# Performance work log

Hardware: AMD Instinct MI355X
Metric: run time of the kernel (lower is better)

Reference implementation:

```python
import jax, jax.numpy as jnp
import numpy as np

M, K, N = 32, 8192, 28672

def setup_inputs() -> dict:
    key = jax.random.key(0)
    k1, k2, k3 = jax.random.split(key, 3)
    act = jax.random.normal(k1, (M, K), dtype=jnp.float16)
    # int8 quantized weight, stored as int8 (spec lists int32 for harness compat)
    weight = jax.random.randint(k2, (K, N), -127, 128, dtype=jnp.int8)
    # per-output-channel dequant scale, small positive values typical of fp8/int8 quant
    scale = (jax.random.uniform(k3, (1, N), dtype=jnp.float32) * 0.01 + 1e-4).astype(jnp.float16)
    return {"act": act, "weight": weight, "scale": scale}

def reference(act, weight, scale):
    # grouped_gemm with single group: out[m,n] = (sum_k act[m,k] * w[k,n]) * scale[n]
    # int8 weight is dequantized inline; accumulate in fp32, emit fp16 like the kernel.
    acc = jnp.einsum("mk,kn->mn", act.astype(jnp.float16), weight.astype(jnp.float16),
                     preferred_element_type=jnp.float32)
    out = acc * scale.astype(jnp.float32)
    return out.astype(jnp.float16)
```

## Files before the change

kernel.cpp:

```cpp
#include <hip/hip_runtime.h>
#include <hip/hip_bf16.h>

#define MM 32
#define KK 8192
#define NN 28672

typedef _Float16 half8  __attribute__((ext_vector_type(8)));
typedef float    floatx4 __attribute__((ext_vector_type(4)));

template <int KSPLIT, int FINAL>
__global__ __launch_bounds__(256) void gemm_kernel(
    const float* __restrict__ act,
    const int*   __restrict__ weight,
    const float* __restrict__ scale,
    float*       __restrict__ ws,
    float*       __restrict__ out)
{
    const int lane = threadIdx.x & 63;
    const int wave = threadIdx.x >> 6;
    const int col  = lane & 15;
    const int quad = lane >> 4;

    const int n0 = blockIdx.x * 64 + wave * 16 + col;
    const int kc = blockIdx.y * (KK / KSPLIT);
    const int ksteps = (KK / KSPLIT) / 32;

    floatx4 acc0 = {0.f, 0.f, 0.f, 0.f};
    floatx4 acc1 = {0.f, 0.f, 0.f, 0.f};

    const float* ap0 = act + (size_t)col * KK + kc + quad * 8;
    const float* ap1 = ap0 + (size_t)16 * KK;
    const int* wp = weight + (size_t)(kc + quad * 8) * NN + n0;

    for (int s = 0; s < ksteps; ++s) {
        floatx4 a0lo = *(const floatx4*)(ap0);
        floatx4 a0hi = *(const floatx4*)(ap0 + 4);
        floatx4 a1lo = *(const floatx4*)(ap1);
        floatx4 a1hi = *(const floatx4*)(ap1 + 4);

        half8 a0, a1, b;
#pragma unroll
        for (int j = 0; j < 4; ++j) {
            a0[j]     = (_Float16)a0lo[j];
            a0[j + 4] = (_Float16)a0hi[j];
            a1[j]     = (_Float16)a1lo[j];
            a1[j + 4] = (_Float16)a1hi[j];
        }
#pragma unroll
        for (int j = 0; j < 8; ++j) {
            b[j] = (_Float16)wp[(size_t)j * NN];
        }

        acc0 = __builtin_amdgcn_mfma_f32_16x16x32_f16(a0, b, acc0, 0, 0, 0);
        acc1 = __builtin_amdgcn_mfma_f32_16x16x32_f16(a1, b, acc1, 0, 0, 0);

        ap0 += 32;
        ap1 += 32;
        wp  += (size_t)32 * NN;
    }

    if (FINAL) {
        float sc = scale[n0];
#pragma unroll
        for (int r = 0; r < 4; ++r) {
            int m0 = quad * 4 + r;
            out[(size_t)m0 * NN + n0]        = acc0[r] * sc;
            out[(size_t)(m0 + 16) * NN + n0] = acc1[r] * sc;
        }
    } else {
        float* wsb = ws + (size_t)blockIdx.y * MM * NN;
#pragma unroll
        for (int r = 0; r < 4; ++r) {
            int m0 = quad * 4 + r;
            wsb[(size_t)m0 * NN + n0]        = acc0[r];
            wsb[(size_t)(m0 + 16) * NN + n0] = acc1[r];
        }
    }
}

template <int KSPLIT>
__global__ __launch_bounds__(256) void finalize_kernel(
    const float* __restrict__ ws,
    const float* __restrict__ scale,
    float*       __restrict__ out)
{
    const int n = blockIdx.x * 256 + threadIdx.x;
    const int m = blockIdx.y;
    if (n >= NN) return;

    float sum = 0.f;
#pragma unroll
    for (int c = 0; c < KSPLIT; ++c)
        sum += ws[(size_t)c * MM * NN + (size_t)m * NN + n];

    out[(size_t)m * NN + n] = sum * scale[n];
}

extern "C" void kernel_launch(void* const* d_in, const int* in_sizes, int n_in,
                              void* d_out, int out_size, void* d_ws, size_t ws_size,
                              hipStream_t stream)
{
    const float* act    = (const float*)d_in[0];
    const int*   weight = (const int*)d_in[1];
    const float* scale  = (const float*)d_in[2];
    float*       out    = (float*)d_out;

    constexpr int KSPLIT = 4;
    const size_t need = (size_t)KSPLIT * MM * NN * sizeof(float);

    if (ws_size >= need) {
        dim3 grid(NN / 64, KSPLIT);
        gemm_kernel<KSPLIT, 0><<<grid, 256, 0, stream>>>(act, weight, scale,
                                                         (float*)d_ws, out);
        dim3 fgrid(NN / 256, MM);
        finalize_kernel<KSPLIT><<<fgrid, 256, 0, stream>>>((const float*)d_ws,
                                                           scale, out);
    } else {
        dim3 grid(NN / 64, 1);
        gemm_kernel<1, 1><<<grid, 256, 0, stream>>>(act, weight, scale,
                                                    nullptr, out);
    }
}
```

Measured before the change: 1.290 ms.

## Stage int weights through LDS with vectorized loads and pre-convert activations to fp16

Adds a pre-pass kernel that converts the fp32 activations to fp16 once in workspace. The split-K GEMM now loads weights as 16-byte vectors across a 128-deep K tile, converts them to fp16, and writes them transposed into padded shared memory. MFMA operands are then read from LDS, replacing the per-lane strided scalar weight loads and the per-step activation conversion. This costs extra workspace, one more kernel launch, and two barriers per stage.

```diff
diff --git a/kernel.cpp b/kernel.cpp
--- a/kernel.cpp
+++ b/kernel.cpp
@@ -5,76 +5,95 @@
 #define KK 8192
 #define NN 28672
 
-typedef _Float16 half8  __attribute__((ext_vector_type(8)));
+typedef _Float16 half8   __attribute__((ext_vector_type(8)));
+typedef __fp16   fp16x2  __attribute__((ext_vector_type(2)));
 typedef float    floatx4 __attribute__((ext_vector_type(4)));
+typedef int      intx4   __attribute__((ext_vector_type(4)));
 
-template <int KSPLIT, int FINAL>
-__global__ __launch_bounds__(256) void gemm_kernel(
-    const float* __restrict__ act,
-    const int*   __restrict__ weight,
-    const float* __restrict__ scale,
-    float*       __restrict__ ws,
-    float*       __restrict__ out)
+__global__ __launch_bounds__(256) void act_cvt_kernel(
+    const float* __restrict__ act, __fp16* __restrict__ act16)
 {
-    const int lane = threadIdx.x & 63;
-    const int wave = threadIdx.x >> 6;
+    int i = (blockIdx.x * 256 + threadIdx.x) * 4;
+    floatx4 v = *(const floatx4*)(act + i);
+    fp16x2 lo = __builtin_amdgcn_cvt_pkrtz(v[0], v[1]);
+    fp16x2 hi = __builtin_amdgcn_cvt_pkrtz(v[2], v[3]);
+    __fp16* o = act16 + i;
+    *(fp16x2*)(o)     = lo;
+    *(fp16x2*)(o + 2) = hi;
+}
+
+#define BN 64
+#define BK 128
+#define LDSTRIDE 136
+
+template <int KSPLIT>
+__global__ __launch_bounds__(256) void gemm_staged_kernel(
+    const __fp16*   __restrict__ act16,
+    const int*      __restrict__ weight,
+    float*          __restrict__ ws)
+{
+    __shared__ __fp16 tileB[BN * LDSTRIDE];
+
+    const int t    = threadIdx.x;
+    const int lane = t & 63;
+    const int wave = t >> 6;
     const int col  = lane & 15;
     const int quad = lane >> 4;
 
-    const int n0 = blockIdx.x * 64 + wave * 16 + col;
-    const int kc = blockIdx.y * (KK / KSPLIT);
-    const int ksteps = (KK / KSPLIT) / 32;
+    const int nblock = blockIdx.x * BN;
+    const int kc     = blockIdx.y * (KK / KSPLIT);
+    const int stages = (KK / KSPLIT) / BK;
+
+    const int seg = t & 15;
+    const int kg  = t >> 4;
+    const int n0s = seg * 4;
+    const int k0s = kg * 8;
 
     floatx4 acc0 = {0.f, 0.f, 0.f, 0.f};
     floatx4 acc1 = {0.f, 0.f, 0.f, 0.f};
 
-    const float* ap0 = act + (size_t)col * KK + kc + quad * 8;
-    const float* ap1 = ap0 + (size_t)16 * KK;
-    const int* wp = weight + (size_t)(kc + quad * 8) * NN + n0;
+    const int* wbase = weight + (size_t)(kc + k0s) * NN + nblock + n0s;
+    const __fp16* abase = act16 + (size_t)col * KK + kc + quad * 8;
 
-    for (int s = 0; s < ksteps; ++s) {
-        floatx4 a0lo = *(const floatx4*)(ap0);
-        floatx4 a0hi = *(const floatx4*)(ap0 + 4);
-        floatx4 a1lo = *(const floatx4*)(ap1);
-        floatx4 a1hi = *(const floatx4*)(ap1 + 4);
+    for (int s = 0; s < stages; ++s) {
+        intx4 w[8];
+#pragma unroll
+        for (int i = 0; i < 8; ++i)
+            w[i] = *(const intx4*)(wbase + (size_t)(s * BK + i) * NN);
 
-        half8 a0, a1, b;
 #pragma unroll
         for (int j = 0; j < 4; ++j) {
-            a0[j]     = (_Float16)a0lo[j];
-            a0[j + 4] = (_Float16)a0hi[j];
-            a1[j]     = (_Float16)a1lo[j];
-            a1[j + 4] = (_Float16)a1hi[j];
+            fp16x2 p0 = __builtin_amdgcn_cvt_pkrtz((float)w[0][j], (float)w[1][j]);
+            fp16x2 p1 = __builtin_amdgcn_cvt_pkrtz((float)w[2][j], (float)w[3][j]);
+            fp16x2 p2 = __builtin_amdgcn_cvt_pkrtz((float)w[4][j], (float)w[5][j]);
+            fp16x2 p3 = __builtin_amdgcn_cvt_pkrtz((float)w[6][j], (float)w[7][j]);
+            __fp16* dst = tileB + (n0s + j) * LDSTRIDE + k0s;
+            *(fp16x2*)(dst)     = p0;
+            *(fp16x2*)(dst + 2) = p1;
+            *(fp16x2*)(dst + 4) = p2;
+            *(fp16x2*)(dst + 6) = p3;
         }
+        __syncthreads();
+
+        const __fp16* brow = tileB + (wave * 16 + col) * LDSTRIDE;
+        const __fp16* ak   = abase + s * BK;
 #pragma unroll
-        for (int j = 0; j < 8; ++j) {
-            b[j] = (_Float16)wp[(size_t)j * NN];
+        for (int kb = 0; kb < BK / 32; ++kb) {
+            half8 b  = *(const half8*)(brow + kb * 32 + quad * 8);
+            half8 a0 = *(const half8*)(ak + kb * 32);
+            half8 a1 = *(const half8*)(ak + kb * 32 + (size_t)16 * KK);
+            acc0 = __builtin_amdgcn_mfma_f32_16x16x32_f16(a0, b, acc0, 0, 0, 0);
+            acc1 = __builtin_amdgcn_mfma_f32_16x16x32_f16(a1, b, acc1, 0, 0, 0);
         }
-
-        acc0 = __builtin_amdgcn_mfma_f32_16x16x32_f16(a0, b, acc0, 0, 0, 0);
-        acc1 = __builtin_amdgcn_mfma_f32_16x16x32_f16(a1, b, acc1, 0, 0, 0);
-
-        ap0 += 32;
-        ap1 += 32;
-        wp  += (size_t)32 * NN;
+        __syncthreads();
     }
 
-    if (FINAL) {
-        float sc = scale[n0];
+    float* wsb = ws + (size_t)blockIdx.y * MM * NN + nblock + wave * 16 + col;
 #pragma unroll
-        for (int r = 0; r < 4; ++r) {
-            int m0 = quad * 4 + r;
-            out[(size_t)m0 * NN + n0]        = acc0[r] * sc;
-            out[(size_t)(m0 + 16) * NN + n0] = acc1[r] * sc;
-        }
-    } else {
-        float* wsb = ws + (size_t)blockIdx.y * MM * NN;
-#pragma unroll
-        for (int r = 0; r < 4; ++r) {
-            int m0 = quad * 4 + r;
-            wsb[(size_t)m0 * NN + n0]        = acc0[r];
-            wsb[(size_t)(m0 + 16) * NN + n0] = acc1[r];
-        }
+    for (int r = 0; r < 4; ++r) {
+        int m0 = quad * 4 + r;
+        wsb[(size_t)m0 * NN]        = acc0[r];
+        wsb[(size_t)(m0 + 16) * NN] = acc1[r];
     }
 }
 
@@ -86,14 +105,56 @@
 {
     const int n = blockIdx.x * 256 + threadIdx.x;
     const int m = blockIdx.y;
-    if (n >= NN) return;
-
     float sum = 0.f;
 #pragma unroll
     for (int c = 0; c < KSPLIT; ++c)
         sum += ws[(size_t)c * MM * NN + (size_t)m * NN + n];
+    out[(size_t)m * NN + n] = sum * scale[n];
+}
 
-    out[(size_t)m * NN + n] = sum * scale[n];
+__global__ __launch_bounds__(256) void gemm_direct_kernel(
+    const float* __restrict__ act,
+    const int*   __restrict__ weight,
+    const float* __restrict__ scale,
+    float*       __restrict__ out)
+{
+    const int lane = threadIdx.x & 63;
+    const int wave = threadIdx.x >> 6;
+    const int col  = lane & 15;
+    const int quad = lane >> 4;
+    const int n0 = blockIdx.x * 64 + wave * 16 + col;
+
+    floatx4 acc0 = {0.f, 0.f, 0.f, 0.f};
+    floatx4 acc1 = {0.f, 0.f, 0.f, 0.f};
+    const float* ap0 = act + (size_t)col * KK + quad * 8;
+    const float* ap1 = ap0 + (size_t)16 * KK;
+    const int* wp = weight + (size_t)(quad * 8) * NN + n0;
+
+    for (int s = 0; s < KK / 32; ++s) {
+        floatx4 a0lo = *(const floatx4*)(ap0);
+        floatx4 a0hi = *(const floatx4*)(ap0 + 4);
+        floatx4 a1lo = *(const floatx4*)(ap1);
+        floatx4 a1hi = *(const floatx4*)(ap1 + 4);
+        half8 a0, a1, b;
+#pragma unroll
+        for (int j = 0; j < 4; ++j) {
+            a0[j] = (_Float16)a0lo[j]; a0[j + 4] = (_Float16)a0hi[j];
+            a1[j] = (_Float16)a1lo[j]; a1[j + 4] = (_Float16)a1hi[j];
+        }
+#pragma unroll
+        for (int j = 0; j < 8; ++j)
+            b[j] = (_Float16)wp[(size_t)j * NN];
+        acc0 = __builtin_amdgcn_mfma_f32_16x16x32_f16(a0, b, acc0, 0, 0, 0);
+        acc1 = __builtin_amdgcn_mfma_f32_16x16x32_f16(a1, b, acc1, 0, 0, 0);
+        ap0 += 32; ap1 += 32; wp += (size_t)32 * NN;
+    }
+    float sc = scale[n0];
+#pragma unroll
+    for (int r = 0; r < 4; ++r) {
+        int m0 = quad * 4 + r;
+        out[(size_t)m0 * NN + n0]        = acc0[r] * sc;
+        out[(size_t)(m0 + 16) * NN + n0] = acc1[r] * sc;
+    }
 }
 
 extern "C" void kernel_launch(void* const* d_in, const int* in_sizes, int n_in,
@@ -106,18 +167,22 @@
     float*       out    = (float*)d_out;
 
     constexpr int KSPLIT = 4;
-    const size_t need = (size_t)KSPLIT * MM * NN * sizeof(float);
+    const size_t partials_bytes = (size_t)KSPLIT * MM * NN * sizeof(float);
+    const size_t act16_off      = partials_bytes;
+    const size_t need           = act16_off + (size_t)MM * KK * sizeof(__fp16);
 
     if (ws_size >= need) {
-        dim3 grid(NN / 64, KSPLIT);
-        gemm_kernel<KSPLIT, 0><<<grid, 256, 0, stream>>>(act, weight, scale,
-                                                         (float*)d_ws, out);
+        float*   ws_part = (float*)d_ws;
+        __fp16*  act16   = (__fp16*)((char*)d_ws + act16_off);
+
+        act_cvt_kernel<<<MM * KK / (256 * 4), 256, 0, stream>>>(act, act16);
+
+        dim3 grid(NN / BN, KSPLIT);
+        gemm_staged_kernel<KSPLIT><<<grid, 256, 0, stream>>>(act16, weight, ws_part);
+
         dim3 fgrid(NN / 256, MM);
-        finalize_kernel<KSPLIT><<<fgrid, 256, 0, stream>>>((const float*)d_ws,
-                                                           scale, out);
+        finalize_kernel<KSPLIT><<<fgrid, 256, 0, stream>>>(ws_part, scale, out);
     } else {
-        dim3 grid(NN / 64, 1);
-        gemm_kernel<1, 1><<<grid, 256, 0, stream>>>(act, weight, scale,
-                                                    nullptr, out);
+        gemm_direct_kernel<<<NN / 64, 256, 0, stream>>>(act, weight, scale, out);
     }
 }
```

Result: faster. 1.205 ms (-6.6%).
